# Performance work log

Hardware: AMD Instinct MI355X
Metric: run time of the kernel (lower is better)

## Reference

```python
import jax, jax.numpy as jnp
import numpy as np

BS, T, ND, DS, IN, H = 512, 100, 10, 6, 256, 256
SA = IN * ND + H  # 2816, attention MLP width


def setup_inputs() -> dict:
    key = jax.random.key(0)
    ks = jax.random.split(key, 8)
    def lin(k, out_d, in_d):
        return jax.random.normal(k, (out_d, in_d), jnp.float32) * (1.0 / np.sqrt(in_d)).astype(np.float32)
    return {
        "descriptors": jax.random.normal(ks[0], (BS, T, ND, DS), jnp.float32),
        "Wd": lin(ks[1], IN, DS), "bd": jnp.zeros((IN,), jnp.float32),
        "W1": lin(ks[2], SA, SA), "b1": jnp.zeros((SA,), jnp.float32),
        "W2": lin(ks[3], IN, SA), "b2": jnp.zeros((IN,), jnp.float32),
        "Wv": lin(ks[4], ND, SA), "bv": jnp.zeros((ND,), jnp.float32),
        "W_ih": lin(ks[5], 4 * H, IN), "W_hh": lin(ks[6], 4 * H, H),
        "b_ih": jnp.zeros((4 * H,), jnp.float32), "b_hh": jnp.zeros((4 * H,), jnp.float32),
    }


def reference(descriptors, Wd, bd, W1, b1, W2, b2, Wv, bv, W_ih, W_hh, b_ih, b_hh):
    bs = descriptors.shape[0]
    dt = descriptors.dtype
    desc_tm = jnp.swapaxes(descriptors, 0, 1)  # [T, bs, ND, DS] time-major for scan
    h0 = jnp.zeros((bs, H), dt)
    c0 = jnp.zeros((bs, H), dt)
    inp0 = jnp.zeros((bs, IN), dt)

    def step(carry, d):
        h, c, inp = carry
        # torch.nn.LSTMCell: gate order i, f, g, o
        gates = inp @ W_ih.T + b_ih + h @ W_hh.T + b_hh  # [bs, 4H]
        i, f, g, o = jnp.split(gates, 4, axis=-1)
        c = jax.nn.sigmoid(f) * c + jax.nn.sigmoid(i) * jnp.tanh(g)
        h = jax.nn.sigmoid(o) * jnp.tanh(c)
        # FrameAttention
        emb = d @ Wd.T + bd                               # [bs, ND, IN]
        x = jnp.concatenate([emb.reshape(bs, ND * IN), h], axis=-1)  # [bs, SA]
        x = jax.nn.relu(x @ W1.T + b1)
        nxt = jax.nn.relu(x @ W2.T + b2)
        a = x @ Wv.T + bv  # training mode: no sigmoid
        return (h, c, nxt), a

    _, att = jax.lax.scan(step, (h0, c0, inp0), desc_tm)  # att: [T, bs, ND]
    return jnp.swapaxes(att, 0, 1)  # [bs, T, ND]
```

## Files before the change

kernel.cpp:

```cpp
#include <hip/hip_runtime.h>
#include <hip/hip_bf16.h>
#include <math.h>

#define TT 100
#define ND 10
#define DS 6
#define SAW 2816

typedef _Float16 half8 __attribute__((ext_vector_type(8)));
typedef float floatx4 __attribute__((ext_vector_type(4)));

__device__ __forceinline__ void gload_lds16(const _Float16* g, _Float16* l) {
    __builtin_amdgcn_global_load_lds((const __attribute__((address_space(1))) void*)g,
                                     (__attribute__((address_space(3))) void*)l, 16, 0, 0);
}

__global__ __launch_bounds__(256) void gemm_big(
    const _Float16* __restrict__ Ah, const _Float16* __restrict__ Al, int lda,
    const _Float16* __restrict__ Bh, const _Float16* __restrict__ Bl, int ldb,
    float* __restrict__ Cpart, size_t zstride, int ldc, int Kloc)
{
    __shared__ alignas(16) _Float16 lds[4 * 128 * 32];

    const int tid = threadIdx.x;
    const int w = tid >> 6, l = tid & 63;
    const int m0 = blockIdx.x * 128, n0 = blockIdx.y * 128;
    const int koff = blockIdx.z * Kloc;

    const _Float16* plane_src;
    int plane_ld;
    if (w == 0)      { plane_src = Ah + (size_t)m0 * lda; plane_ld = lda; }
    else if (w == 1) { plane_src = Al + (size_t)m0 * lda; plane_ld = lda; }
    else if (w == 2) { plane_src = Bh + (size_t)n0 * ldb; plane_ld = ldb; }
    else             { plane_src = Bl + (size_t)n0 * ldb; plane_ld = ldb; }
    const int srow_in_chunk = l >> 2;
    const int scol = (l & 3) * 8;
    _Float16* const lds_plane = lds + w * 4096;

    const int wr = (w >> 1) * 64, wc = (w & 1) * 64;
    const int fr = l & 15, fk = (l >> 4) * 8;

    floatx4 acc[4][4];
    const floatx4 z4 = {0.f, 0.f, 0.f, 0.f};
#pragma unroll
    for (int i = 0; i < 4; ++i)
#pragma unroll
        for (int j = 0; j < 4; ++j) acc[i][j] = z4;

    for (int kt = 0; kt < Kloc; kt += 32) {
        __syncthreads();
#pragma unroll
        for (int i = 0; i < 8; ++i) {
            const int row = i * 16 + srow_in_chunk;
            gload_lds16(plane_src + (size_t)row * plane_ld + koff + kt + scol,
                        lds_plane + i * 512);
        }
        __syncthreads();

        half8 aH[4], aL[4], bH[4], bL[4];
#pragma unroll
        for (int f = 0; f < 4; ++f) {
            const int ra = (wr + f * 16 + fr) * 32 + fk;
            const int rb = (wc + f * 16 + fr) * 32 + fk;
            aH[f] = *(const half8*)&lds[ra];
            aL[f] = *(const half8*)&lds[4096 + ra];
            bH[f] = *(const half8*)&lds[8192 + rb];
            bL[f] = *(const half8*)&lds[12288 + rb];
        }
#pragma unroll
        for (int mf = 0; mf < 4; ++mf)
#pragma unroll
            for (int nf = 0; nf < 4; ++nf)
                acc[mf][nf] = __builtin_amdgcn_mfma_f32_16x16x32_f16(aH[mf], bH[nf], acc[mf][nf], 0, 0, 0);
#pragma unroll
        for (int mf = 0; mf < 4; ++mf)
#pragma unroll
            for (int nf = 0; nf < 4; ++nf)
                acc[mf][nf] = __builtin_amdgcn_mfma_f32_16x16x32_f16(aH[mf], bL[nf], acc[mf][nf], 0, 0, 0);
#pragma unroll
        for (int mf = 0; mf < 4; ++mf)
#pragma unroll
            for (int nf = 0; nf < 4; ++nf)
                acc[mf][nf] = __builtin_amdgcn_mfma_f32_16x16x32_f16(aL[mf], bH[nf], acc[mf][nf], 0, 0, 0);
    }

    float* const Cz = Cpart + (size_t)blockIdx.z * zstride;
    const int cr = (l >> 4) * 4, cc = l & 15;
#pragma unroll
    for (int mf = 0; mf < 4; ++mf) {
        const int row = m0 + wr + mf * 16 + cr;
#pragma unroll
        for (int nf = 0; nf < 4; ++nf) {
            const int col = n0 + wc + nf * 16 + cc;
#pragma unroll
            for (int r = 0; r < 4; ++r)
                Cz[(size_t)(row + r) * ldc + col] = acc[mf][nf][r];
        }
    }
}

__global__ __launch_bounds__(256) void gemm_s16_part(
    const _Float16* __restrict__ Ah, const _Float16* __restrict__ Al, int lda,
    const _Float16* __restrict__ Bh, const _Float16* __restrict__ Bl, int ldb,
    float* __restrict__ Cf, int ldc, int Kloc)
{
    __shared__ alignas(16) _Float16 sAh[64 * 32];
    __shared__ alignas(16) _Float16 sAl[64 * 32];
    __shared__ alignas(16) _Float16 sBh[64 * 32];
    __shared__ alignas(16) _Float16 sBl[64 * 32];

    const int tid = threadIdx.x;
    const int w = tid >> 6, l = tid & 63;
    const int m0 = blockIdx.x * 64, n0 = blockIdx.y * 64;
    const int koff = blockIdx.z * Kloc;

    const int sr = 16 * w + (l >> 2);
    const int sc = (l & 3) * 8;
    const int sidx = sr * 32 + sc;
    const _Float16* gAh = Ah + (size_t)(m0 + sr) * lda + koff + sc;
    const _Float16* gAl = Al + (size_t)(m0 + sr) * lda + koff + sc;
    const _Float16* gBh = Bh + (size_t)(n0 + sr) * ldb + koff + sc;
    const _Float16* gBl = Bl + (size_t)(n0 + sr) * ldb + koff + sc;

    const int mw = (w >> 1) * 32, nw = (w & 1) * 32;
    const int fr = l & 15, fk = (l >> 4) * 8;

    floatx4 acc[2][2];
    const floatx4 z = {0.f, 0.f, 0.f, 0.f};
#pragma unroll
    for (int i = 0; i < 2; ++i)
#pragma unroll
        for (int j = 0; j < 2; ++j) acc[i][j] = z;

    half8 rAh = *(const half8*)gAh;
    half8 rAl = *(const half8*)gAl;
    half8 rBh = *(const half8*)gBh;
    half8 rBl = *(const half8*)gBl;

    for (int kt = 0; kt < Kloc; kt += 32) {
        *(half8*)&sAh[sidx] = rAh;
        *(half8*)&sAl[sidx] = rAl;
        *(half8*)&sBh[sidx] = rBh;
        *(half8*)&sBl[sidx] = rBl;
        __syncthreads();
        if (kt + 32 < Kloc) {
            rAh = *(const half8*)(gAh + kt + 32);
            rAl = *(const half8*)(gAl + kt + 32);
            rBh = *(const half8*)(gBh + kt + 32);
            rBl = *(const half8*)(gBl + kt + 32);
        }
        half8 aH[2], aL[2], bH[2], bL[2];
#pragma unroll
        for (int mf = 0; mf < 2; ++mf) {
            const int ro = (mw + mf * 16 + fr) * 32 + fk;
            aH[mf] = *(const half8*)&sAh[ro];
            aL[mf] = *(const half8*)&sAl[ro];
        }
#pragma unroll
        for (int nf = 0; nf < 2; ++nf) {
            const int ro = (nw + nf * 16 + fr) * 32 + fk;
            bH[nf] = *(const half8*)&sBh[ro];
            bL[nf] = *(const half8*)&sBl[ro];
        }
#pragma unroll
        for (int mf = 0; mf < 2; ++mf)
#pragma unroll
            for (int nf = 0; nf < 2; ++nf)
                acc[mf][nf] = __builtin_amdgcn_mfma_f32_16x16x32_f16(aH[mf], bH[nf], acc[mf][nf], 0, 0, 0);
#pragma unroll
        for (int mf = 0; mf < 2; ++mf)
#pragma unroll
            for (int nf = 0; nf < 2; ++nf)
                acc[mf][nf] = __builtin_amdgcn_mfma_f32_16x16x32_f16(aH[mf], bL[nf], acc[mf][nf], 0, 0, 0);
#pragma unroll
        for (int mf = 0; mf < 2; ++mf)
#pragma unroll
            for (int nf = 0; nf < 2; ++nf)
                acc[mf][nf] = __builtin_amdgcn_mfma_f32_16x16x32_f16(aL[mf], bH[nf], acc[mf][nf], 0, 0, 0);
        __syncthreads();
    }

    const int cr = (l >> 4) * 4, cc = l & 15;
#pragma unroll
    for (int nf = 0; nf < 2; ++nf) {
        const int col = n0 + nw + nf * 16 + cc;
#pragma unroll
        for (int mf = 0; mf < 2; ++mf) {
            const int row = m0 + mw + mf * 16 + cr;
#pragma unroll
            for (int r = 0; r < 4; ++r)
                Cf[(size_t)blockIdx.z * (512 * 256) + (size_t)(row + r) * ldc + col]
                    = acc[mf][nf][r];
        }
    }
}

__global__ __launch_bounds__(256) void yred(const float* __restrict__ pbufY,
                                            const float* __restrict__ b1,
                                            _Float16* __restrict__ yhi,
                                            _Float16* __restrict__ ylo)
{
    const int b = blockIdx.x, tid = threadIdx.x;
    for (int i = tid; i < SAW; i += 256) {
        float s = b1[i];
#pragma unroll
        for (int z = 0; z < 4; ++z) s += pbufY[(size_t)z * 1441792 + (size_t)b * SAW + i];
        s = s > 0.f ? s : 0.f;
        const _Float16 h = (_Float16)s;
        yhi[(size_t)b * SAW + i] = h;
        ylo[(size_t)b * SAW + i] = (_Float16)(s - (float)h);
    }
}

__global__ __launch_bounds__(256) void lstm_emb(
    const float* __restrict__ gpart, const float* __restrict__ b_ih,
    const float* __restrict__ b_hh, float* __restrict__ cbuf,
    _Float16* __restrict__ zhi, _Float16* __restrict__ zlo,
    _Float16* __restrict__ xhi, _Float16* __restrict__ xlo,
    const float* __restrict__ desc, const float* __restrict__ Wd,
    const float* __restrict__ bd, int t)
{
    __shared__ float sd[60];
    __shared__ float swd[1536];
    const int b = blockIdx.x, k = threadIdx.x;
    if (k < 60) sd[k] = desc[(size_t)b * (TT * ND * DS) + t * (ND * DS) + k];
    for (int i = k; i < 1536; i += 256) swd[i] = Wd[i];

    float gate[4];
#pragma unroll
    for (int g = 0; g < 4; ++g) {
        const int idx = g * 256 + k;
        float s = b_ih[idx] + b_hh[idx];
#pragma unroll
        for (int z = 0; z < 4; ++z) s += gpart[z * 524288 + b * 1024 + idx];
        gate[g] = s;
    }
    const float si = 1.f / (1.f + expf(-gate[0]));
    const float sf = 1.f / (1.f + expf(-gate[1]));
    const float so = 1.f / (1.f + expf(-gate[3]));
    float cv = cbuf[b * 256 + k];
    cv = sf * cv + si * tanhf(gate[2]);
    const float hv = so * tanhf(cv);
    cbuf[b * 256 + k] = cv;
    {
        const _Float16 h = (_Float16)hv;
        const _Float16 lo = (_Float16)(hv - (float)h);
        zhi[b * 512 + 256 + k] = h;   zlo[b * 512 + 256 + k] = lo;
        xhi[(size_t)b * SAW + 2560 + k] = h;
        xlo[(size_t)b * SAW + 2560 + k] = lo;
    }
    __syncthreads();

    const float bdv = bd[k];
#pragma unroll
    for (int n = 0; n < ND; ++n) {
        float a = bdv;
#pragma unroll
        for (int d = 0; d < DS; ++d) a += sd[n * DS + d] * swd[k * DS + d];
        const _Float16 h = (_Float16)a;
        xhi[(size_t)b * SAW + n * 256 + k] = h;
        xlo[(size_t)b * SAW + n * 256 + k] = (_Float16)(a - (float)h);
    }
}

__global__ __launch_bounds__(256) void av_w2fin(
    const _Float16* __restrict__ yhi, const _Float16* __restrict__ ylo,
    const float* __restrict__ Wv, const float* __restrict__ bv,
    const float* __restrict__ pbuf, const float* __restrict__ b2,
    _Float16* __restrict__ zhi, _Float16* __restrict__ zlo,
    float* __restrict__ out, int t)
{
    __shared__ float ys[SAW];
    __shared__ float red[ND][4];
    const int b = blockIdx.x, tid = threadIdx.x;
    for (int i = tid; i < SAW; i += 256)
        ys[i] = (float)yhi[(size_t)b * SAW + i] + (float)ylo[(size_t)b * SAW + i];
    __syncthreads();

    float pacc[ND];
#pragma unroll
    for (int n = 0; n < ND; ++n) pacc[n] = 0.f;
    for (int kk = tid; kk < SAW; kk += 256) {
        const float yv = ys[kk];
#pragma unroll
        for (int n = 0; n < ND; ++n) pacc[n] += yv * Wv[n * SAW + kk];
    }
    const int lane = tid & 63, wid = tid >> 6;
#pragma unroll
    for (int n = 0; n < ND; ++n) {
        float v = pacc[n];
        for (int off = 32; off > 0; off >>= 1) v += __shfl_down(v, off, 64);
        if (lane == 0) red[n][wid] = v;
    }
    {
        const int j = tid;
        float s = b2[j];
#pragma unroll
        for (int kc = 0; kc < 4; ++kc) s += pbuf[kc * 131072 + b * 256 + j];
        s = s > 0.f ? s : 0.f;
        const _Float16 h = (_Float16)s;
        zhi[b * 512 + j] = h;
        zlo[b * 512 + j] = (_Float16)(s - (float)h);
    }
    __syncthreads();
    if (tid < ND) {
        const float s = red[tid][0] + red[tid][1] + red[tid][2] + red[tid][3] + bv[tid];
        out[(size_t)b * (TT * ND) + t * ND + tid] = s;
    }
}

__global__ void build_wcat_split(const float* __restrict__ W_ih, const float* __restrict__ W_hh,
                                 _Float16* __restrict__ wchi, _Float16* __restrict__ wclo)
{
    const int j = blockIdx.x, k = threadIdx.x;
    const float v1 = W_ih[j * 256 + k];
    const _Float16 h1 = (_Float16)v1;
    wchi[j * 512 + k] = h1;
    wclo[j * 512 + k] = (_Float16)(v1 - (float)h1);
    const float v2 = W_hh[j * 256 + k];
    const _Float16 h2 = (_Float16)v2;
    wchi[j * 512 + 256 + k] = h2;
    wclo[j * 512 + 256 + k] = (_Float16)(v2 - (float)h2);
}

__global__ __launch_bounds__(256) void cvt_hilo(const float* __restrict__ src,
                                                _Float16* __restrict__ hi,
                                                _Float16* __restrict__ lo, int n)
{
    int i = blockIdx.x * 256 + threadIdx.x;
    const int stride = gridDim.x * 256;
    for (; i < n; i += stride) {
        const float v = src[i];
        const _Float16 h = (_Float16)v;
        hi[i] = h;
        lo[i] = (_Float16)(v - (float)h);
    }
}

extern "C" void kernel_launch(void* const* d_in, const int* in_sizes, int n_in,
                              void* d_out, int out_size, void* d_ws, size_t ws_size,
                              hipStream_t stream)
{
    const float* desc = (const float*)d_in[0];
    const float* Wd   = (const float*)d_in[1];
    const float* bd   = (const float*)d_in[2];
    const float* W1   = (const float*)d_in[3];
    const float* b1   = (const float*)d_in[4];
    const float* W2   = (const float*)d_in[5];
    const float* b2   = (const float*)d_in[6];
    const float* Wv   = (const float*)d_in[7];
    const float* bv   = (const float*)d_in[8];
    const float* W_ih = (const float*)d_in[9];
    const float* W_hh = (const float*)d_in[10];
    const float* b_ih = (const float*)d_in[11];
    const float* b_hh = (const float*)d_in[12];
    float* out = (float*)d_out;

    char* ws = (char*)d_ws;
    _Float16* zhi  = (_Float16*)(ws);
    _Float16* zlo  = (_Float16*)(ws + 524288);
    float*    cbuf = (float*)(ws + 1048576);
    _Float16* xhi  = (_Float16*)(ws + 1572864);
    _Float16* xlo  = (_Float16*)(ws + 4456448);
    _Float16* yhi  = xhi;
    _Float16* ylo  = xlo;
    float*    gpart = (float*)(ws + 7340032);
    float*    pbufY = (float*)(ws + 7340032);
    float*    pbufW2= (float*)(ws + 7340032);
    _Float16* wchi = (_Float16*)(ws + 30408704);
    _Float16* wclo = (_Float16*)(ws + 31457280);
    _Float16* w2hi = (_Float16*)(ws + 32505856);
    _Float16* w2lo = (_Float16*)(ws + 33947648);
    _Float16* w1hi = (_Float16*)(ws + 35389440);
    _Float16* w1lo = (_Float16*)(ws + 51249152);

    hipMemsetAsync(ws, 0, 1572864, stream);
    build_wcat_split<<<dim3(1024), dim3(256), 0, stream>>>(W_ih, W_hh, wchi, wclo);
    cvt_hilo<<<dim3(4096), dim3(256), 0, stream>>>(W1, w1hi, w1lo, SAW * SAW);
    cvt_hilo<<<dim3(704), dim3(256), 0, stream>>>(W2, w2hi, w2lo, 256 * SAW);

    for (int t = 0; t < TT; ++t) {
        gemm_big<<<dim3(4, 8, 4), dim3(256), 0, stream>>>(
            zhi, zlo, 512, wchi, wclo, 512, gpart, 524288, 1024, 128);
        lstm_emb<<<dim3(512), dim3(256), 0, stream>>>(gpart, b_ih, b_hh, cbuf,
                                                      zhi, zlo, xhi, xlo,
                                                      desc, Wd, bd, t);
        gemm_big<<<dim3(4, 22, 4), dim3(256), 0, stream>>>(
            xhi, xlo, SAW, w1hi, w1lo, SAW, pbufY, 1441792, SAW, 704);
        yred<<<dim3(512), dim3(256), 0, stream>>>(pbufY, b1, yhi, ylo);
        gemm_s16_part<<<dim3(8, 4, 4), dim3(256), 0, stream>>>(
            yhi, ylo, SAW, w2hi, w2lo, SAW, pbufW2, 256, 704);
        av_w2fin<<<dim3(512), dim3(256), 0, stream>>>(yhi, ylo, Wv, bv, pbufW2, b2,
                                                      zhi, zlo, out, t);
    }
}
```

Measured before the change: 8.738 ms.

## Fuse LSTM gates with cell update and fold split-K reductions into atomic GEMM epilogues

Restructures the per-timestep pipeline from six kernels down to four. The LSTM gate GEMM is fused with the cell update and the embedding, using gate-interleaved weights so each block owns complete i/f/g/o groups. The h-part of the gates is precomputed after h is updated. The W1 and W2 split-K GEMMs now accumulate with atomics, and a last-block counter applies bias, ReLU and the hi/lo split, which removes the separate reduction kernels. Wv is appended to W2 as extra output columns, so the attention output comes out of the same GEMM. This trades fewer launches and less partial-buffer traffic for atomic contention and extra fences.

```diff
diff --git a/kernel.cpp b/kernel.cpp
--- a/kernel.cpp
+++ b/kernel.cpp
@@ -15,24 +15,246 @@
                                      (__attribute__((address_space(3))) void*)l, 16, 0, 0);
 }
 
-__global__ __launch_bounds__(256) void gemm_big(
-    const _Float16* __restrict__ Ah, const _Float16* __restrict__ Al, int lda,
-    const _Float16* __restrict__ Bh, const _Float16* __restrict__ Bl, int ldb,
-    float* __restrict__ Cpart, size_t zstride, int ldc, int Kloc)
+__global__ __launch_bounds__(256) void gates_lstm_emb(
+    const _Float16* __restrict__ zrhi, const _Float16* __restrict__ zrlo,
+    const _Float16* __restrict__ wihhi, const _Float16* __restrict__ wihlo,
+    const float* __restrict__ ghh,
+    const float* __restrict__ b_ih, const float* __restrict__ b_hh,
+    float* __restrict__ cbuf,
+    _Float16* __restrict__ zwhi, _Float16* __restrict__ zwlo,
+    _Float16* __restrict__ xhi, _Float16* __restrict__ xlo,
+    const float* __restrict__ desc, const float* __restrict__ Wd,
+    const float* __restrict__ bd, int t)
+{
+    __shared__ alignas(16) _Float16 sAh[64 * 32];
+    __shared__ alignas(16) _Float16 sAl[64 * 32];
+    __shared__ alignas(16) _Float16 sBh[64 * 32];
+    __shared__ alignas(16) _Float16 sBl[64 * 32];
+    __shared__ float sg[64][68];
+
+    const int tid = threadIdx.x, w = tid >> 6, l = tid & 63;
+    const int m0 = blockIdx.x * 64, n0 = blockIdx.y * 64;
+    const int sr = 16 * w + (l >> 2), sc = (l & 3) * 8, sidx = sr * 32 + sc;
+    const _Float16* gAh = zrhi + (size_t)(m0 + sr) * 512 + sc;
+    const _Float16* gAl = zrlo + (size_t)(m0 + sr) * 512 + sc;
+    const _Float16* gBh = wihhi + (size_t)(n0 + sr) * 256 + sc;
+    const _Float16* gBl = wihlo + (size_t)(n0 + sr) * 256 + sc;
+    const int mw = (w >> 1) * 32, nw = (w & 1) * 32;
+    const int fr = l & 15, fk = (l >> 4) * 8;
+    const int cr = (l >> 4) * 4, cc = l & 15;
+
+    floatx4 acc[2][2];
+#pragma unroll
+    for (int mf = 0; mf < 2; ++mf)
+#pragma unroll
+        for (int nf = 0; nf < 2; ++nf)
+#pragma unroll
+            for (int r = 0; r < 4; ++r)
+                acc[mf][nf][r] = ghh[(size_t)(m0 + mw + mf * 16 + cr + r) * 1024
+                                     + (n0 + nw + nf * 16 + cc)];
+
+    half8 rAh = *(const half8*)gAh;
+    half8 rAl = *(const half8*)gAl;
+    half8 rBh = *(const half8*)gBh;
+    half8 rBl = *(const half8*)gBl;
+
+    for (int kt = 0; kt < 256; kt += 32) {
+        *(half8*)&sAh[sidx] = rAh;
+        *(half8*)&sAl[sidx] = rAl;
+        *(half8*)&sBh[sidx] = rBh;
+        *(half8*)&sBl[sidx] = rBl;
+        __syncthreads();
+        if (kt + 32 < 256) {
+            rAh = *(const half8*)(gAh + kt + 32);
+            rAl = *(const half8*)(gAl + kt + 32);
+            rBh = *(const half8*)(gBh + kt + 32);
+            rBl = *(const half8*)(gBl + kt + 32);
+        }
+        half8 aH[2], aL[2], bH[2], bL[2];
+#pragma unroll
+        for (int mf = 0; mf < 2; ++mf) {
+            const int ro = (mw + mf * 16 + fr) * 32 + fk;
+            aH[mf] = *(const half8*)&sAh[ro];
+            aL[mf] = *(const half8*)&sAl[ro];
+        }
+#pragma unroll
+        for (int nf = 0; nf < 2; ++nf) {
+            const int ro = (nw + nf * 16 + fr) * 32 + fk;
+            bH[nf] = *(const half8*)&sBh[ro];
+            bL[nf] = *(const half8*)&sBl[ro];
+        }
+#pragma unroll
+        for (int mf = 0; mf < 2; ++mf)
+#pragma unroll
+            for (int nf = 0; nf < 2; ++nf)
+                acc[mf][nf] = __builtin_amdgcn_mfma_f32_16x16x32_f16(aH[mf], bH[nf], acc[mf][nf], 0, 0, 0);
+#pragma unroll
+        for (int mf = 0; mf < 2; ++mf)
+#pragma unroll
+            for (int nf = 0; nf < 2; ++nf)
+                acc[mf][nf] = __builtin_amdgcn_mfma_f32_16x16x32_f16(aH[mf], bL[nf], acc[mf][nf], 0, 0, 0);
+#pragma unroll
+        for (int mf = 0; mf < 2; ++mf)
+#pragma unroll
+            for (int nf = 0; nf < 2; ++nf)
+                acc[mf][nf] = __builtin_amdgcn_mfma_f32_16x16x32_f16(aL[mf], bH[nf], acc[mf][nf], 0, 0, 0);
+        __syncthreads();
+    }
+
+#pragma unroll
+    for (int mf = 0; mf < 2; ++mf)
+#pragma unroll
+        for (int nf = 0; nf < 2; ++nf)
+#pragma unroll
+            for (int r = 0; r < 4; ++r)
+                sg[mw + mf * 16 + cr + r][nw + nf * 16 + cc] = acc[mf][nf][r];
+    __syncthreads();
+
+    const int q0 = blockIdx.y * 16;
+#pragma unroll
+    for (int it = 0; it < 4; ++it) {
+        const int idx = it * 256 + tid;
+        const int r_ = idx >> 4, ch = idx & 15;
+        const int b = m0 + r_, gq = q0 + ch;
+        const float gi = sg[r_][4 * ch + 0] + b_ih[gq]       + b_hh[gq];
+        const float gf = sg[r_][4 * ch + 1] + b_ih[256 + gq] + b_hh[256 + gq];
+        const float gg = sg[r_][4 * ch + 2] + b_ih[512 + gq] + b_hh[512 + gq];
+        const float go = sg[r_][4 * ch + 3] + b_ih[768 + gq] + b_hh[768 + gq];
+        const float si = 1.f / (1.f + expf(-gi));
+        const float sf = 1.f / (1.f + expf(-gf));
+        const float so = 1.f / (1.f + expf(-go));
+        float cv = cbuf[b * 256 + gq];
+        cv = sf * cv + si * tanhf(gg);
+        const float hv = so * tanhf(cv);
+        cbuf[b * 256 + gq] = cv;
+        const _Float16 h = (_Float16)hv;
+        const _Float16 lo = (_Float16)(hv - (float)h);
+        zwhi[b * 512 + 256 + gq] = h;
+        zwlo[b * 512 + 256 + gq] = lo;
+        xhi[(size_t)b * SAW + 2560 + gq] = h;
+        xlo[(size_t)b * SAW + 2560 + gq] = lo;
+    }
+
+    const int c0 = blockIdx.y * 160;
+    for (int idx = tid; idx < 64 * 160; idx += 256) {
+        const int r_ = idx / 160, c = c0 + idx % 160;
+        const int b = m0 + r_, n = c >> 8, i = c & 255;
+        float a = bd[i];
+        const float* dp = desc + ((size_t)b * TT + t) * 60 + n * 6;
+#pragma unroll
+        for (int d = 0; d < 6; ++d) a += dp[d] * Wd[i * 6 + d];
+        const _Float16 h = (_Float16)a;
+        xhi[(size_t)b * SAW + c] = h;
+        xlo[(size_t)b * SAW + c] = (_Float16)(a - (float)h);
+    }
+}
+
+__global__ __launch_bounds__(256) void ghh_gemm(
+    const _Float16* __restrict__ zhi, const _Float16* __restrict__ zlo,
+    const _Float16* __restrict__ whhhi, const _Float16* __restrict__ whhlo,
+    float* __restrict__ ghh)
+{
+    __shared__ alignas(16) _Float16 sAh[64 * 32];
+    __shared__ alignas(16) _Float16 sAl[64 * 32];
+    __shared__ alignas(16) _Float16 sBh[64 * 32];
+    __shared__ alignas(16) _Float16 sBl[64 * 32];
+
+    const int tid = threadIdx.x, w = tid >> 6, l = tid & 63;
+    const int m0 = blockIdx.x * 64, n0 = blockIdx.y * 64;
+    const int sr = 16 * w + (l >> 2), sc = (l & 3) * 8, sidx = sr * 32 + sc;
+    const _Float16* gAh = zhi + (size_t)(m0 + sr) * 512 + 256 + sc;
+    const _Float16* gAl = zlo + (size_t)(m0 + sr) * 512 + 256 + sc;
+    const _Float16* gBh = whhhi + (size_t)(n0 + sr) * 256 + sc;
+    const _Float16* gBl = whhlo + (size_t)(n0 + sr) * 256 + sc;
+    const int mw = (w >> 1) * 32, nw = (w & 1) * 32;
+    const int fr = l & 15, fk = (l >> 4) * 8;
+
+    floatx4 acc[2][2];
+    const floatx4 z4 = {0.f, 0.f, 0.f, 0.f};
+#pragma unroll
+    for (int i = 0; i < 2; ++i)
+#pragma unroll
+        for (int j = 0; j < 2; ++j) acc[i][j] = z4;
+
+    half8 rAh = *(const half8*)gAh;
+    half8 rAl = *(const half8*)gAl;
+    half8 rBh = *(const half8*)gBh;
+    half8 rBl = *(const half8*)gBl;
+
+    for (int kt = 0; kt < 256; kt += 32) {
+        *(half8*)&sAh[sidx] = rAh;
+        *(half8*)&sAl[sidx] = rAl;
+        *(half8*)&sBh[sidx] = rBh;
+        *(half8*)&sBl[sidx] = rBl;
+        __syncthreads();
+        if (kt + 32 < 256) {
+            rAh = *(const half8*)(gAh + kt + 32);
+            rAl = *(const half8*)(gAl + kt + 32);
+            rBh = *(const half8*)(gBh + kt + 32);
+            rBl = *(const half8*)(gBl + kt + 32);
+        }
+        half8 aH[2], aL[2], bH[2], bL[2];
+#pragma unroll
+        for (int mf = 0; mf < 2; ++mf) {
+            const int ro = (mw + mf * 16 + fr) * 32 + fk;
+            aH[mf] = *(const half8*)&sAh[ro];
+            aL[mf] = *(const half8*)&sAl[ro];
+        }
+#pragma unroll
+        for (int nf = 0; nf < 2; ++nf) {
+            const int ro = (nw + nf * 16 + fr) * 32 + fk;
+            bH[nf] = *(const half8*)&sBh[ro];
+            bL[nf] = *(const half8*)&sBl[ro];
+        }
+#pragma unroll
+        for (int mf = 0; mf < 2; ++mf)
+#pragma unroll
+            for (int nf = 0; nf < 2; ++nf)
+                acc[mf][nf] = __builtin_amdgcn_mfma_f32_16x16x32_f16(aH[mf], bH[nf], acc[mf][nf], 0, 0, 0);
+#pragma unroll
+        for (int mf = 0; mf < 2; ++mf)
+#pragma unroll
+            for (int nf = 0; nf < 2; ++nf)
+                acc[mf][nf] = __builtin_amdgcn_mfma_f32_16x16x32_f16(aH[mf], bL[nf], acc[mf][nf], 0, 0, 0);
+#pragma unroll
+        for (int mf = 0; mf < 2; ++mf)
+#pragma unroll
+            for (int nf = 0; nf < 2; ++nf)
+                acc[mf][nf] = __builtin_amdgcn_mfma_f32_16x16x32_f16(aL[mf], bH[nf], acc[mf][nf], 0, 0, 0);
+        __syncthreads();
+    }
+
+    const int cr = (l >> 4) * 4, cc = l & 15;
+#pragma unroll
+    for (int mf = 0; mf < 2; ++mf)
+#pragma unroll
+        for (int nf = 0; nf < 2; ++nf)
+#pragma unroll
+            for (int r = 0; r < 4; ++r)
+                ghh[(size_t)(m0 + mw + mf * 16 + cr + r) * 1024
+                    + (n0 + nw + nf * 16 + cc)] = acc[mf][nf][r];
+}
+
+__global__ __launch_bounds__(256) void w1_atomic(
+    const _Float16* __restrict__ Ah, const _Float16* __restrict__ Al,
+    const _Float16* __restrict__ Bh, const _Float16* __restrict__ Bl,
+    float* __restrict__ ybuf, const float* __restrict__ b1,
+    _Float16* __restrict__ yhi, _Float16* __restrict__ ylo,
+    int* __restrict__ ctr)
 {
     __shared__ alignas(16) _Float16 lds[4 * 128 * 32];
+    __shared__ int isLast;
 
     const int tid = threadIdx.x;
     const int w = tid >> 6, l = tid & 63;
     const int m0 = blockIdx.x * 128, n0 = blockIdx.y * 128;
-    const int koff = blockIdx.z * Kloc;
+    const int koff = blockIdx.z * 704;
 
     const _Float16* plane_src;
-    int plane_ld;
-    if (w == 0)      { plane_src = Ah + (size_t)m0 * lda; plane_ld = lda; }
-    else if (w == 1) { plane_src = Al + (size_t)m0 * lda; plane_ld = lda; }
-    else if (w == 2) { plane_src = Bh + (size_t)n0 * ldb; plane_ld = ldb; }
-    else             { plane_src = Bl + (size_t)n0 * ldb; plane_ld = ldb; }
+    if (w == 0)      plane_src = Ah + (size_t)m0 * SAW;
+    else if (w == 1) plane_src = Al + (size_t)m0 * SAW;
+    else if (w == 2) plane_src = Bh + (size_t)n0 * SAW;
+    else             plane_src = Bl + (size_t)n0 * SAW;
     const int srow_in_chunk = l >> 2;
     const int scol = (l & 3) * 8;
     _Float16* const lds_plane = lds + w * 4096;
@@ -47,12 +269,12 @@
 #pragma unroll
         for (int j = 0; j < 4; ++j) acc[i][j] = z4;
 
-    for (int kt = 0; kt < Kloc; kt += 32) {
+    for (int kt = 0; kt < 704; kt += 32) {
         __syncthreads();
 #pragma unroll
         for (int i = 0; i < 8; ++i) {
             const int row = i * 16 + srow_in_chunk;
-            gload_lds16(plane_src + (size_t)row * plane_ld + koff + kt + scol,
+            gload_lds16(plane_src + (size_t)row * SAW + koff + kt + scol,
                         lds_plane + i * 512);
         }
         __syncthreads();
@@ -84,7 +306,6 @@
                 acc[mf][nf] = __builtin_amdgcn_mfma_f32_16x16x32_f16(aL[mf], bH[nf], acc[mf][nf], 0, 0, 0);
     }
 
-    float* const Cz = Cpart + (size_t)blockIdx.z * zstride;
     const int cr = (l >> 4) * 4, cc = l & 15;
 #pragma unroll
     for (int mf = 0; mf < 4; ++mf) {
@@ -94,56 +315,79 @@
             const int col = n0 + wc + nf * 16 + cc;
 #pragma unroll
             for (int r = 0; r < 4; ++r)
-                Cz[(size_t)(row + r) * ldc + col] = acc[mf][nf][r];
-        }
-    }
-}
-
-__global__ __launch_bounds__(256) void gemm_s16_part(
-    const _Float16* __restrict__ Ah, const _Float16* __restrict__ Al, int lda,
-    const _Float16* __restrict__ Bh, const _Float16* __restrict__ Bl, int ldb,
-    float* __restrict__ Cf, int ldc, int Kloc)
+                atomicAdd(&ybuf[(size_t)(row + r) * SAW + col], acc[mf][nf][r]);
+        }
+    }
+    __threadfence();
+    if (tid == 0) {
+        const int old = atomicAdd(&ctr[blockIdx.y * 4 + blockIdx.x], 1);
+        isLast = ((old & 3) == 3);
+    }
+    __syncthreads();
+    if (isLast) {
+        __threadfence();
+#pragma unroll
+        for (int k = 0; k < 64; ++k) {
+            const int idx = k * 256 + tid;
+            const int row = m0 + (idx >> 7), col = n0 + (idx & 127);
+            const size_t o = (size_t)row * SAW + col;
+            float s = ybuf[o];
+            ybuf[o] = 0.f;
+            float v = s + b1[col];
+            v = v > 0.f ? v : 0.f;
+            const _Float16 h = (_Float16)v;
+            yhi[o] = h;
+            ylo[o] = (_Float16)(v - (float)h);
+        }
+    }
+}
+
+__global__ __launch_bounds__(256) void w2v_atomic(
+    const _Float16* __restrict__ yhi, const _Float16* __restrict__ ylo,
+    const _Float16* __restrict__ Bh, const _Float16* __restrict__ Bl,
+    float* __restrict__ w2acc, const float* __restrict__ b2,
+    const float* __restrict__ bv,
+    _Float16* __restrict__ zhi, _Float16* __restrict__ zlo,
+    float* __restrict__ out, int* __restrict__ ctr, int t)
 {
     __shared__ alignas(16) _Float16 sAh[64 * 32];
     __shared__ alignas(16) _Float16 sAl[64 * 32];
     __shared__ alignas(16) _Float16 sBh[64 * 32];
     __shared__ alignas(16) _Float16 sBl[64 * 32];
-
-    const int tid = threadIdx.x;
-    const int w = tid >> 6, l = tid & 63;
+    __shared__ int isLast;
+
+    const int tid = threadIdx.x, w = tid >> 6, l = tid & 63;
     const int m0 = blockIdx.x * 64, n0 = blockIdx.y * 64;
-    const int koff = blockIdx.z * Kloc;
-
-    const int sr = 16 * w + (l >> 2);
-    const int sc = (l & 3) * 8;
-    const int sidx = sr * 32 + sc;
-    const _Float16* gAh = Ah + (size_t)(m0 + sr) * lda + koff + sc;
-    const _Float16* gAl = Al + (size_t)(m0 + sr) * lda + koff + sc;
-    const _Float16* gBh = Bh + (size_t)(n0 + sr) * ldb + koff + sc;
-    const _Float16* gBl = Bl + (size_t)(n0 + sr) * ldb + koff + sc;
-
+    const int koff = blockIdx.z * 704;
+
+    const int sr = 16 * w + (l >> 2), sc = (l & 3) * 8, sidx = sr * 32 + sc;
+    const int brow = min(n0 + sr, 271);
+    const _Float16* gAh = yhi + (size_t)(m0 + sr) * SAW + koff + sc;
+    const _Float16* gAl = ylo + (size_t)(m0 + sr) * SAW + koff + sc;
+    const _Float16* gBh = Bh + (size_t)brow * SAW + koff + sc;
+    const _Float16* gBl = Bl + (size_t)brow * SAW + koff + sc;
     const int mw = (w >> 1) * 32, nw = (w & 1) * 32;
     const int fr = l & 15, fk = (l >> 4) * 8;
 
     floatx4 acc[2][2];
-    const floatx4 z = {0.f, 0.f, 0.f, 0.f};
+    const floatx4 z4 = {0.f, 0.f, 0.f, 0.f};
 #pragma unroll
     for (int i = 0; i < 2; ++i)
 #pragma unroll
-        for (int j = 0; j < 2; ++j) acc[i][j] = z;
+        for (int j = 0; j < 2; ++j) acc[i][j] = z4;
 
     half8 rAh = *(const half8*)gAh;
     half8 rAl = *(const half8*)gAl;
     half8 rBh = *(const half8*)gBh;
     half8 rBl = *(const half8*)gBl;
 
-    for (int kt = 0; kt < Kloc; kt += 32) {
+    for (int kt = 0; kt < 704; kt += 32) {
         *(half8*)&sAh[sidx] = rAh;
         *(half8*)&sAl[sidx] = rAl;
         *(half8*)&sBh[sidx] = rBh;
         *(half8*)&sBl[sidx] = rBl;
         __syncthreads();
-        if (kt + 32 < Kloc) {
+        if (kt + 32 < 704) {
             rAh = *(const half8*)(gAh + kt + 32);
             rAl = *(const half8*)(gAl + kt + 32);
             rBh = *(const half8*)(gBh + kt + 32);
@@ -189,138 +433,66 @@
             const int row = m0 + mw + mf * 16 + cr;
 #pragma unroll
             for (int r = 0; r < 4; ++r)
-                Cf[(size_t)blockIdx.z * (512 * 256) + (size_t)(row + r) * ldc + col]
-                    = acc[mf][nf][r];
-        }
-    }
-}
-
-__global__ __launch_bounds__(256) void yred(const float* __restrict__ pbufY,
-                                            const float* __restrict__ b1,
-                                            _Float16* __restrict__ yhi,
-                                            _Float16* __restrict__ ylo)
-{
-    const int b = blockIdx.x, tid = threadIdx.x;
-    for (int i = tid; i < SAW; i += 256) {
-        float s = b1[i];
-#pragma unroll
-        for (int z = 0; z < 4; ++z) s += pbufY[(size_t)z * 1441792 + (size_t)b * SAW + i];
-        s = s > 0.f ? s : 0.f;
-        const _Float16 h = (_Float16)s;
-        yhi[(size_t)b * SAW + i] = h;
-        ylo[(size_t)b * SAW + i] = (_Float16)(s - (float)h);
-    }
-}
-
-__global__ __launch_bounds__(256) void lstm_emb(
-    const float* __restrict__ gpart, const float* __restrict__ b_ih,
-    const float* __restrict__ b_hh, float* __restrict__ cbuf,
-    _Float16* __restrict__ zhi, _Float16* __restrict__ zlo,
-    _Float16* __restrict__ xhi, _Float16* __restrict__ xlo,
-    const float* __restrict__ desc, const float* __restrict__ Wd,
-    const float* __restrict__ bd, int t)
-{
-    __shared__ float sd[60];
-    __shared__ float swd[1536];
-    const int b = blockIdx.x, k = threadIdx.x;
-    if (k < 60) sd[k] = desc[(size_t)b * (TT * ND * DS) + t * (ND * DS) + k];
-    for (int i = k; i < 1536; i += 256) swd[i] = Wd[i];
-
-    float gate[4];
-#pragma unroll
-    for (int g = 0; g < 4; ++g) {
-        const int idx = g * 256 + k;
-        float s = b_ih[idx] + b_hh[idx];
-#pragma unroll
-        for (int z = 0; z < 4; ++z) s += gpart[z * 524288 + b * 1024 + idx];
-        gate[g] = s;
-    }
-    const float si = 1.f / (1.f + expf(-gate[0]));
-    const float sf = 1.f / (1.f + expf(-gate[1]));
-    const float so = 1.f / (1.f + expf(-gate[3]));
-    float cv = cbuf[b * 256 + k];
-    cv = sf * cv + si * tanhf(gate[2]);
-    const float hv = so * tanhf(cv);
-    cbuf[b * 256 + k] = cv;
-    {
-        const _Float16 h = (_Float16)hv;
-        const _Float16 lo = (_Float16)(hv - (float)h);
-        zhi[b * 512 + 256 + k] = h;   zlo[b * 512 + 256 + k] = lo;
-        xhi[(size_t)b * SAW + 2560 + k] = h;
-        xlo[(size_t)b * SAW + 2560 + k] = lo;
+                atomicAdd(&w2acc[(row + r) * 320 + col], acc[mf][nf][r]);
+        }
+    }
+    __threadfence();
+    if (tid == 0) {
+        const int old = atomicAdd(&ctr[blockIdx.y * 8 + blockIdx.x], 1);
+        isLast = ((old & 3) == 3);
     }
     __syncthreads();
-
-    const float bdv = bd[k];
-#pragma unroll
-    for (int n = 0; n < ND; ++n) {
-        float a = bdv;
-#pragma unroll
-        for (int d = 0; d < DS; ++d) a += sd[n * DS + d] * swd[k * DS + d];
-        const _Float16 h = (_Float16)a;
-        xhi[(size_t)b * SAW + n * 256 + k] = h;
-        xlo[(size_t)b * SAW + n * 256 + k] = (_Float16)(a - (float)h);
-    }
-}
-
-__global__ __launch_bounds__(256) void av_w2fin(
-    const _Float16* __restrict__ yhi, const _Float16* __restrict__ ylo,
-    const float* __restrict__ Wv, const float* __restrict__ bv,
-    const float* __restrict__ pbuf, const float* __restrict__ b2,
-    _Float16* __restrict__ zhi, _Float16* __restrict__ zlo,
-    float* __restrict__ out, int t)
-{
-    __shared__ float ys[SAW];
-    __shared__ float red[ND][4];
-    const int b = blockIdx.x, tid = threadIdx.x;
-    for (int i = tid; i < SAW; i += 256)
-        ys[i] = (float)yhi[(size_t)b * SAW + i] + (float)ylo[(size_t)b * SAW + i];
-    __syncthreads();
-
-    float pacc[ND];
-#pragma unroll
-    for (int n = 0; n < ND; ++n) pacc[n] = 0.f;
-    for (int kk = tid; kk < SAW; kk += 256) {
-        const float yv = ys[kk];
-#pragma unroll
-        for (int n = 0; n < ND; ++n) pacc[n] += yv * Wv[n * SAW + kk];
-    }
-    const int lane = tid & 63, wid = tid >> 6;
-#pragma unroll
-    for (int n = 0; n < ND; ++n) {
-        float v = pacc[n];
-        for (int off = 32; off > 0; off >>= 1) v += __shfl_down(v, off, 64);
-        if (lane == 0) red[n][wid] = v;
-    }
-    {
-        const int j = tid;
-        float s = b2[j];
-#pragma unroll
-        for (int kc = 0; kc < 4; ++kc) s += pbuf[kc * 131072 + b * 256 + j];
-        s = s > 0.f ? s : 0.f;
-        const _Float16 h = (_Float16)s;
-        zhi[b * 512 + j] = h;
-        zlo[b * 512 + j] = (_Float16)(s - (float)h);
-    }
-    __syncthreads();
-    if (tid < ND) {
-        const float s = red[tid][0] + red[tid][1] + red[tid][2] + red[tid][3] + bv[tid];
-        out[(size_t)b * (TT * ND) + t * ND + tid] = s;
-    }
-}
-
-__global__ void build_wcat_split(const float* __restrict__ W_ih, const float* __restrict__ W_hh,
-                                 _Float16* __restrict__ wchi, _Float16* __restrict__ wclo)
+    if (isLast) {
+        __threadfence();
+#pragma unroll
+        for (int k = 0; k < 16; ++k) {
+            const int idx = k * 256 + tid;
+            const int row = m0 + (idx >> 6), col = n0 + (idx & 63);
+            float s = w2acc[row * 320 + col];
+            w2acc[row * 320 + col] = 0.f;
+            if (col < 256) {
+                float v = s + b2[col];
+                v = v > 0.f ? v : 0.f;
+                const _Float16 h = (_Float16)v;
+                zhi[row * 512 + col] = h;
+                zlo[row * 512 + col] = (_Float16)(v - (float)h);
+            } else if (col < 266) {
+                out[(size_t)row * (TT * ND) + t * ND + (col - 256)] = s + bv[col - 256];
+            }
+        }
+    }
+}
+
+__global__ void build_ilv(const float* __restrict__ W_ih, const float* __restrict__ W_hh,
+                          _Float16* __restrict__ wihhi, _Float16* __restrict__ wihlo,
+                          _Float16* __restrict__ whhhi, _Float16* __restrict__ whhlo)
 {
     const int j = blockIdx.x, k = threadIdx.x;
-    const float v1 = W_ih[j * 256 + k];
-    const _Float16 h1 = (_Float16)v1;
-    wchi[j * 512 + k] = h1;
-    wclo[j * 512 + k] = (_Float16)(v1 - (float)h1);
-    const float v2 = W_hh[j * 256 + k];
-    const _Float16 h2 = (_Float16)v2;
-    wchi[j * 512 + 256 + k] = h2;
-    wclo[j * 512 + 256 + k] = (_Float16)(v2 - (float)h2);
+    const int orow = (j & 3) * 256 + (j >> 2);
+    float v = W_ih[orow * 256 + k];
+    _Float16 h = (_Float16)v;
+    wihhi[j * 256 + k] = h;
+    wihlo[j * 256 + k] = (_Float16)(v - (float)h);
+    v = W_hh[orow * 256 + k];
+    h = (_Float16)v;
+    whhhi[j * 256 + k] = h;
+    whhlo[j * 256 + k] = (_Float16)(v - (float)h);
+}
+
+__global__ __launch_bounds__(256) void build_w2v(const float* __restrict__ W2,
+                                                 const float* __restrict__ Wv,
+                                                 _Float16* __restrict__ hi,
+                                                 _Float16* __restrict__ lo)
+{
+    const int j = blockIdx.x;
+    for (int k = threadIdx.x; k < SAW; k += 256) {
+        float v = 0.f;
+        if (j < 256)       v = W2[(size_t)j * SAW + k];
+        else if (j < 266)  v = Wv[(size_t)(j - 256) * SAW + k];
+        const _Float16 h = (_Float16)v;
+        hi[(size_t)j * SAW + k] = h;
+        lo[(size_t)j * SAW + k] = (_Float16)(v - (float)h);
+    }
 }
 
 __global__ __launch_bounds__(256) void cvt_hilo(const float* __restrict__ src,
@@ -357,40 +529,41 @@
     float* out = (float*)d_out;
 
     char* ws = (char*)d_ws;
-    _Float16* zhi  = (_Float16*)(ws);
-    _Float16* zlo  = (_Float16*)(ws + 524288);
-    float*    cbuf = (float*)(ws + 1048576);
-    _Float16* xhi  = (_Float16*)(ws + 1572864);
-    _Float16* xlo  = (_Float16*)(ws + 4456448);
-    _Float16* yhi  = xhi;
-    _Float16* ylo  = xlo;
-    float*    gpart = (float*)(ws + 7340032);
-    float*    pbufY = (float*)(ws + 7340032);
-    float*    pbufW2= (float*)(ws + 7340032);
-    _Float16* wchi = (_Float16*)(ws + 30408704);
-    _Float16* wclo = (_Float16*)(ws + 31457280);
-    _Float16* w2hi = (_Float16*)(ws + 32505856);
-    _Float16* w2lo = (_Float16*)(ws + 33947648);
-    _Float16* w1hi = (_Float16*)(ws + 35389440);
-    _Float16* w1lo = (_Float16*)(ws + 51249152);
+    _Float16* zhi   = (_Float16*)(ws);
+    _Float16* zlo   = (_Float16*)(ws + 524288);
+    float*    cbuf  = (float*)(ws + 1048576);
+    _Float16* xhi   = (_Float16*)(ws + 1572864);
+    _Float16* xlo   = (_Float16*)(ws + 4456448);
+    float*    ybuf  = (float*)(ws + 7340032);
+    float*    w2acc = (float*)(ws + 13107200);
+    float*    ghh   = (float*)(ws + 13762560);
+    int*      ctrY  = (int*)(ws + 15859712);
+    int*      ctrW2 = (int*)(ws + 15860064);
+    _Float16* wihhi = (_Float16*)(ws + 15860224);
+    _Float16* wihlo = (_Float16*)(ws + 16384512);
+    _Float16* whhhi = (_Float16*)(ws + 16908800);
+    _Float16* whhlo = (_Float16*)(ws + 17433088);
+    _Float16* w2vhi = (_Float16*)(ws + 17957376);
+    _Float16* w2vlo = (_Float16*)(ws + 19489280);
+    _Float16* w1hi  = (_Float16*)(ws + 21021184);
+    _Float16* w1lo  = (_Float16*)(ws + 36880896);
+    _Float16* yhi   = (_Float16*)(ws + 52740608);
+    _Float16* ylo   = (_Float16*)(ws + 55624192);
 
     hipMemsetAsync(ws, 0, 1572864, stream);
-    build_wcat_split<<<dim3(1024), dim3(256), 0, stream>>>(W_ih, W_hh, wchi, wclo);
+    hipMemsetAsync(ws + 7340032, 0, 15860224 - 7340032, stream);
+    build_ilv<<<dim3(1024), dim3(256), 0, stream>>>(W_ih, W_hh, wihhi, wihlo, whhhi, whhlo);
+    build_w2v<<<dim3(272), dim3(256), 0, stream>>>(W2, Wv, w2vhi, w2vlo);
     cvt_hilo<<<dim3(4096), dim3(256), 0, stream>>>(W1, w1hi, w1lo, SAW * SAW);
-    cvt_hilo<<<dim3(704), dim3(256), 0, stream>>>(W2, w2hi, w2lo, 256 * SAW);
 
     for (int t = 0; t < TT; ++t) {
-        gemm_big<<<dim3(4, 8, 4), dim3(256), 0, stream>>>(
-            zhi, zlo, 512, wchi, wclo, 512, gpart, 524288, 1024, 128);
-        lstm_emb<<<dim3(512), dim3(256), 0, stream>>>(gpart, b_ih, b_hh, cbuf,
-                                                      zhi, zlo, xhi, xlo,
-                                                      desc, Wd, bd, t);
-        gemm_big<<<dim3(4, 22, 4), dim3(256), 0, stream>>>(
-            xhi, xlo, SAW, w1hi, w1lo, SAW, pbufY, 1441792, SAW, 704);
-        yred<<<dim3(512), dim3(256), 0, stream>>>(pbufY, b1, yhi, ylo);
-        gemm_s16_part<<<dim3(8, 4, 4), dim3(256), 0, stream>>>(
-            yhi, ylo, SAW, w2hi, w2lo, SAW, pbufW2, 256, 704);
-        av_w2fin<<<dim3(512), dim3(256), 0, stream>>>(yhi, ylo, Wv, bv, pbufW2, b2,
-                                                      zhi, zlo, out, t);
-    }
-}
+        gates_lstm_emb<<<dim3(8, 16), dim3(256), 0, stream>>>(
+            zhi, zlo, wihhi, wihlo, ghh, b_ih, b_hh, cbuf,
+            zhi, zlo, xhi, xlo, desc, Wd, bd, t);
+        ghh_gemm<<<dim3(8, 16), dim3(256), 0, stream>>>(zhi, zlo, whhhi, whhlo, ghh);
+        w1_atomic<<<dim3(4, 22, 4), dim3(256), 0, stream>>>(
+            xhi, xlo, w1hi, w1lo, ybuf, b1, yhi, ylo, ctrY);
+        w2v_atomic<<<dim3(8, 5, 4), dim3(256), 0, stream>>>(
+            yhi, ylo, w2vhi, w2vlo, w2acc, b2, bv, zhi, zlo, out, ctrW2, t);
+    }
+}
```

Measured after the change: 13.76 ms. 57.5% more time.
